# Optimization experiments

Measured on AMD Instinct MI355X. Metric: run time of the kernel, lower is better.

The kernel has to match this reference:

```python
import jax, jax.numpy as jnp
import numpy as np

N = 50000      # nodes
E = 800000     # edges (avg degree 16)
IN = 128       # in_dim0
H = 96         # hidden_dim
BN_EPS = 1e-5
PN_SCALE = 20.0


def setup_inputs() -> dict:
    key = jax.random.key(0)
    ks = jax.random.split(key, 12)
    s_in = 1.0 / np.sqrt(IN)
    s_h = 1.0 / np.sqrt(H)
    return {
        "x": jax.random.normal(ks[0], (N, IN), jnp.float32),
        "edge_index": jax.random.randint(ks[1], (2, E), 0, N, jnp.int32),
        # mlp0: Linear(in_dim0 -> hidden)
        "W0": jax.random.uniform(ks[2], (H, IN), jnp.float32, -s_in, s_in),
        "b0": jax.random.uniform(ks[3], (H,), jnp.float32, -s_in, s_in),
        # GIN MLP layer 1: Linear(hidden -> hidden) + BatchNorm
        "W1": jax.random.uniform(ks[4], (H, H), jnp.float32, -s_h, s_h),
        "b1": jax.random.uniform(ks[5], (H,), jnp.float32, -s_h, s_h),
        "gamma": jnp.ones((H,), jnp.float32),
        "beta": jnp.zeros((H,), jnp.float32),
        # GIN MLP layer 2: Linear(hidden -> hidden)
        "W2": jax.random.uniform(ks[6], (H, H), jnp.float32, -s_h, s_h),
        "b2": jax.random.uniform(ks[7], (H,), jnp.float32, -s_h, s_h),
    }


def reference(x, edge_index, W0, b0, W1, b1, gamma, beta, W2, b2):
    # h0 = mlp0(x)
    h0 = x @ W0.T + b0                                   # [N, H]

    # GINConv (eps=0): z_i = h0_i + sum_{j->i} h0_j
    src, dst = edge_index[0], edge_index[1]
    agg = jax.ops.segment_sum(h0[src], dst, num_segments=N)  # [N, H]
    z = h0 + agg

    # GIN MLP (layer_num=2): Linear -> BatchNorm(train) -> ReLU -> Linear
    h = z @ W1.T + b1
    mean = h.mean(axis=0)
    var = h.var(axis=0)                                  # biased, like torch BN
    h = (h - mean) * jax.lax.rsqrt(var + BN_EPS) * gamma + beta
    h = jax.nn.relu(h)
    l1 = h @ W2.T + b2                                   # [N, H]

    # PairNorm 'PN-SCS', scale=20
    col_mean = l1.mean(axis=0)
    rownorm = jnp.sqrt(1e-6 + jnp.sum(l1 * l1, axis=1, keepdims=True))
    l1 = PN_SCALE * l1 / rownorm - col_mean

    return (l1, h0)
```

## Files before the change

kernel.cpp:

```cpp
#include <hip/hip_runtime.h>

#define NN 50000
#define IN_DIM 128
#define HD 96
#define BN_EPS 1e-5f
#define PN_SCALE 20.0f
#define SCAN_NB 196
#define NREP 4

using bf16x8 = __attribute__((ext_vector_type(8))) short;
using f32x4  = __attribute__((ext_vector_type(4))) float;

__device__ __forceinline__ float4 ld4(const float* p) { return *(const float4*)p; }
__device__ __forceinline__ float4 add4(float4 a, float4 b) {
    return make_float4(a.x + b.x, a.y + b.y, a.z + b.z, a.w + b.w);
}

__device__ __forceinline__ short bfr(float f) {
    unsigned u = __float_as_uint(f);
    unsigned r = u + 0x7fffu + ((u >> 16) & 1u);
    return (short)(r >> 16);
}
__device__ __forceinline__ bf16x8 cvt8(float4 a, float4 b) {
    bf16x8 r;
    r[0] = bfr(a.x); r[1] = bfr(a.y); r[2] = bfr(a.z); r[3] = bfr(a.w);
    r[4] = bfr(b.x); r[5] = bfr(b.y); r[6] = bfr(b.z); r[7] = bfr(b.w);
    return r;
}

__global__ void zero_kernel(float* stats, int* cnt) {
    int i = blockIdx.x * blockDim.x + threadIdx.x;
    if (i < 1024) stats[i] = 0.0f;
    int j = i - 1024;
    if (j >= 0 && j < NREP * NN) cnt[j] = 0;
}

template<int K, int MODE>
__global__ __launch_bounds__(256) void gemm_mfma(
    const float* A, const float* __restrict__ W, const float* __restrict__ bias,
    float* out, const float* __restrict__ scale, const float* __restrict__ shift,
    float* __restrict__ gsum, float* __restrict__ gsumsq,
    float* __restrict__ gcol, float* __restrict__ growss,
    const int* __restrict__ ei, int* __restrict__ hist_cnt, int E)
{
    constexpr int P     = K + 8;
    constexpr int NS    = K / 32;
    constexpr int KD4   = K / 4;
    constexpr int WITER = (96 * KD4) / 256;
    constexpr int WL_SH  = 96 * P;
    constexpr int WL_TOT = (20608 > WL_SH) ? 20608 : WL_SH;
    __shared__ short Wl[WL_TOT];

    const int t    = threadIdx.x;
    const int l    = t & 63;
    const int w    = t >> 6;
    const int l15  = l & 15;
    const int lh   = l >> 4;
    const int base = blockIdx.x * 64;

    const int  arow = base + w * 16 + l15;
    const bool aok  = arow < NN;
    const float* Ap = A + (size_t)arow * K + lh * 8;
    const float4 Z4 = make_float4(0.f, 0.f, 0.f, 0.f);

    float4 pa[2 * NS];
#pragma unroll
    for (int s = 0; s < NS; ++s) {
        pa[2 * s]     = aok ? ld4(Ap + s * 32)     : Z4;
        pa[2 * s + 1] = aok ? ld4(Ap + s * 32 + 4) : Z4;
    }
    float4 wv[WITER];
#pragma unroll
    for (int i = 0; i < WITER; ++i) {
        int c = t + i * 256;
        int row = c / KD4, kq = c - row * KD4;
        wv[i] = ld4(W + (size_t)row * K + kq * 4);
    }
    float4 scv[2 * NS], shv[2 * NS];
    if (MODE == 2) {
#pragma unroll
        for (int s = 0; s < 2 * NS; ++s) {
            scv[s] = ld4(scale + (s >> 1) * 32 + lh * 8 + (s & 1) * 4);
            shv[s] = ld4(shift + (s >> 1) * 32 + lh * 8 + (s & 1) * 4);
        }
    }

    if (MODE == 0) {
        int e0 = (blockIdx.x * 256 + t) * 4;
        if (e0 + 4 <= E) {
            int4 d4 = *(const int4*)(ei + E + e0);
            atomicAdd(&hist_cnt[0 * NN + d4.x], 1);
            atomicAdd(&hist_cnt[1 * NN + d4.y], 1);
            atomicAdd(&hist_cnt[2 * NN + d4.z], 1);
            atomicAdd(&hist_cnt[3 * NN + d4.w], 1);
        } else {
            for (int i = 0; i < 4; ++i) {
                int e = e0 + i;
                if (e < E) atomicAdd(&hist_cnt[(e & 3) * NN + ei[E + e]], 1);
            }
        }
    }

    bf16x8 af[NS];
#pragma unroll
    for (int s = 0; s < NS; ++s) {
        float4 q0 = pa[2 * s], q1 = pa[2 * s + 1];
        if (MODE == 2) {
            float4 sc0 = scv[2 * s], sh0 = shv[2 * s];
            float4 sc1 = scv[2 * s + 1], sh1 = shv[2 * s + 1];
            q0.x = fmaxf(q0.x * sc0.x + sh0.x, 0.f);
            q0.y = fmaxf(q0.y * sc0.y + sh0.y, 0.f);
            q0.z = fmaxf(q0.z * sc0.z + sh0.z, 0.f);
            q0.w = fmaxf(q0.w * sc0.w + sh0.w, 0.f);
            q1.x = fmaxf(q1.x * sc1.x + sh1.x, 0.f);
            q1.y = fmaxf(q1.y * sc1.y + sh1.y, 0.f);
            q1.z = fmaxf(q1.z * sc1.z + sh1.z, 0.f);
            q1.w = fmaxf(q1.w * sc1.w + sh1.w, 0.f);
        }
        af[s] = cvt8(q0, q1);
    }

#pragma unroll
    for (int i = 0; i < WITER; ++i) {
        int c = t + i * 256;
        int row = c / KD4, kq = c - row * KD4;
        short4 s4v;
        s4v.x = bfr(wv[i].x); s4v.y = bfr(wv[i].y);
        s4v.z = bfr(wv[i].z); s4v.w = bfr(wv[i].w);
        *(short4*)(Wl + row * P + kq * 4) = s4v;
    }
    __syncthreads();

    f32x4 acc[6];
#pragma unroll
    for (int n = 0; n < 6; ++n) acc[n] = (f32x4){0.f, 0.f, 0.f, 0.f};

#pragma unroll
    for (int s = 0; s < NS; ++s) {
        const short* wp = Wl + s * 32 + lh * 8;
#pragma unroll
        for (int n = 0; n < 6; ++n) {
            bf16x8 bf = *(const bf16x8*)(wp + (n * 16 + l15) * P);
            acc[n] = __builtin_amdgcn_mfma_f32_16x16x32_bf16(af[s], bf, acc[n], 0, 0, 0);
        }
    }

    float cv[6][4];
#pragma unroll
    for (int n = 0; n < 6; ++n) {
        float b = bias[n * 16 + l15];
#pragma unroll
        for (int r = 0; r < 4; ++r) cv[n][r] = acc[n][r] + b;
    }
    int crow[4]; bool cok[4];
#pragma unroll
    for (int r = 0; r < 4; ++r) {
        crow[r] = base + w * 16 + lh * 4 + r;
        cok[r]  = crow[r] < NN;
    }
#pragma unroll
    for (int r = 0; r < 4; ++r) {
        if (cok[r]) {
            float* o = out + (size_t)crow[r] * HD + l15;
#pragma unroll
            for (int n = 0; n < 6; ++n) o[n * 16] = cv[n][r];
        }
    }

    if (MODE == 1) {
        float s[6], q[6];
#pragma unroll
        for (int n = 0; n < 6; ++n) {
            s[n] = 0.f; q[n] = 0.f;
#pragma unroll
            for (int r = 0; r < 4; ++r) {
                float v = cok[r] ? cv[n][r] : 0.f;
                s[n] += v; q[n] += v * v;
            }
        }
#pragma unroll
        for (int n = 0; n < 6; ++n) {
            s[n] += __shfl_xor(s[n], 16); s[n] += __shfl_xor(s[n], 32);
            q[n] += __shfl_xor(q[n], 16); q[n] += __shfl_xor(q[n], 32);
        }
        __syncthreads();
        float* red0 = (float*)Wl;
        float* red1 = red0 + 384;
        if (lh == 0) {
#pragma unroll
            for (int n = 0; n < 6; ++n) {
                red0[w * 96 + n * 16 + l15] = s[n];
                red1[w * 96 + n * 16 + l15] = q[n];
            }
        }
        __syncthreads();
        if (t < HD) {
            float S = red0[t] + red0[96 + t] + red0[192 + t] + red0[288 + t];
            float Q = red1[t] + red1[96 + t] + red1[192 + t] + red1[288 + t];
            atomicAdd(&gsum[t], S);
            atomicAdd(&gsumsq[t], Q);
        }
    }

    if (MODE == 2) {
        float s[6];
#pragma unroll
        for (int n = 0; n < 6; ++n) {
            s[n] = 0.f;
#pragma unroll
            for (int r = 0; r < 4; ++r) s[n] += cok[r] ? cv[n][r] : 0.f;
        }
#pragma unroll
        for (int n = 0; n < 6; ++n) {
            s[n] += __shfl_xor(s[n], 16); s[n] += __shfl_xor(s[n], 32);
        }
        float rq[4];
#pragma unroll
        for (int r = 0; r < 4; ++r) {
            float v = 0.f;
#pragma unroll
            for (int n = 0; n < 6; ++n) v = fmaf(cv[n][r], cv[n][r], v);
            v += __shfl_xor(v, 1); v += __shfl_xor(v, 2);
            v += __shfl_xor(v, 4); v += __shfl_xor(v, 8);
            rq[r] = v;
        }
        __syncthreads();
        float* red0 = (float*)Wl;
        if (lh == 0) {
#pragma unroll
            for (int n = 0; n < 6; ++n) red0[w * 96 + n * 16 + l15] = s[n];
        }
        __syncthreads();
        if (t < HD) {
            float S = red0[t] + red0[96 + t] + red0[192 + t] + red0[288 + t];
            atomicAdd(&gcol[t], S);
        }
        if (l15 == 0) {
#pragma unroll
            for (int r = 0; r < 4; ++r)
                if (cok[r]) growss[crow[r]] = rq[r];
        }
    }
}

__global__ __launch_bounds__(256) void scan_part1(const int* __restrict__ cnt,
                                                  int* __restrict__ bsum) {
    __shared__ int sh[256];
    int i = blockIdx.x * 256 + threadIdx.x;
    int t = threadIdx.x;
    int v = 0;
    if (i < NN)
        v = cnt[i] + cnt[NN + i] + cnt[2 * NN + i] + cnt[3 * NN + i];
    sh[t] = v;
    __syncthreads();
    for (int off = 128; off > 0; off >>= 1) {
        if (t < off) sh[t] += sh[t + off];
        __syncthreads();
    }
    if (t == 0) bsum[blockIdx.x] = sh[0];
}

__global__ __launch_bounds__(256) void scan_part2(int* __restrict__ bsum) {
    __shared__ int sh[256];
    int t = threadIdx.x;
    int v = (t < SCAN_NB) ? bsum[t] : 0;
    sh[t] = v;
    __syncthreads();
    for (int off = 1; off < 256; off <<= 1) {
        int u = sh[t];
        if (t >= off) u += sh[t - off];
        __syncthreads();
        sh[t] = u;
        __syncthreads();
    }
    if (t < SCAN_NB) bsum[t] = sh[t] - v;
}

__global__ __launch_bounds__(256) void scan_part3(int* __restrict__ cnt,
                                                  const int* __restrict__ bsum,
                                                  int* __restrict__ rowptr) {
    __shared__ int sh[256];
    int i = blockIdx.x * 256 + threadIdx.x;
    int t = threadIdx.x;
    int c0 = 0, c1 = 0, c2 = 0, c3 = 0;
    if (i < NN) {
        c0 = cnt[i]; c1 = cnt[NN + i]; c2 = cnt[2 * NN + i]; c3 = cnt[3 * NN + i];
    }
    int v = c0 + c1 + c2 + c3;
    sh[t] = v;
    __syncthreads();
    for (int off = 1; off < 256; off <<= 1) {
        int u = sh[t];
        if (t >= off) u += sh[t - off];
        __syncthreads();
        sh[t] = u;
        __syncthreads();
    }
    int excl = sh[t] - v + bsum[blockIdx.x];
    if (i < NN) {
        rowptr[i] = excl;
        cnt[i]          = excl;
        cnt[NN + i]     = excl + c0;
        cnt[2 * NN + i] = excl + c0 + c1;
        cnt[3 * NN + i] = excl + c0 + c1 + c2;
    }
    if (i == NN - 1) rowptr[NN] = excl + v;
}

__global__ __launch_bounds__(256) void fill_kernel(const int* __restrict__ ei,
                                                   int* __restrict__ cursor,
                                                   int* __restrict__ srcs, int E) {
    int t2 = blockIdx.x * 256 + threadIdx.x;
    int e0 = t2 * 2;
    int src[2], dst[2], rep[2];
#pragma unroll
    for (int i = 0; i < 2; ++i) {
        int e = e0 + i;
        bool ok = e < E;
        dst[i] = ok ? ei[E + e] : -1;
        src[i] = ok ? ei[e] : 0;
        rep[i] = e & 3;
    }
    for (int pass = 0; pass < 7; ++pass) {
#pragma unroll
        for (int i = 0; i < 2; ++i) {
            if (dst[i] >= 0 && (dst[i] >> 13) == pass) {
                int slot = atomicAdd(&cursor[rep[i] * NN + dst[i]], 1);
                srcs[slot] = src[i];
            }
        }
    }
}

__global__ __launch_bounds__(192) void gather_kernel(
    const float* __restrict__ h0, const int* __restrict__ rowptr,
    const int* __restrict__ srcs, float* __restrict__ z)
{
    const int tid = threadIdx.x;
    const int rl  = tid / 24;
    const int c   = tid - rl * 24;
    const int row = blockIdx.x * 8 + rl;
    if (row >= NN) return;

    const int p0 = rowptr[row];
    const int p1 = rowptr[row + 1];

    float4 acc = ld4(h0 + (size_t)row * HD + c * 4);

    int p = p0;
    for (; p + 8 <= p1; p += 8) {
        int s0 = srcs[p + 0], s1 = srcs[p + 1], s2 = srcs[p + 2], s3 = srcs[p + 3];
        int s4 = srcs[p + 4], s5 = srcs[p + 5], s6 = srcs[p + 6], s7 = srcs[p + 7];
        float4 v0 = ld4(h0 + (size_t)s0 * HD + c * 4);
        float4 v1 = ld4(h0 + (size_t)s1 * HD + c * 4);
        float4 v2 = ld4(h0 + (size_t)s2 * HD + c * 4);
        float4 v3 = ld4(h0 + (size_t)s3 * HD + c * 4);
        float4 v4 = ld4(h0 + (size_t)s4 * HD + c * 4);
        float4 v5 = ld4(h0 + (size_t)s5 * HD + c * 4);
        float4 v6 = ld4(h0 + (size_t)s6 * HD + c * 4);
        float4 v7 = ld4(h0 + (size_t)s7 * HD + c * 4);
        acc = add4(acc, add4(add4(add4(v0, v1), add4(v2, v3)),
                             add4(add4(v4, v5), add4(v6, v7))));
    }
    for (; p + 4 <= p1; p += 4) {
        int s0 = srcs[p + 0], s1 = srcs[p + 1], s2 = srcs[p + 2], s3 = srcs[p + 3];
        float4 v0 = ld4(h0 + (size_t)s0 * HD + c * 4);
        float4 v1 = ld4(h0 + (size_t)s1 * HD + c * 4);
        float4 v2 = ld4(h0 + (size_t)s2 * HD + c * 4);
        float4 v3 = ld4(h0 + (size_t)s3 * HD + c * 4);
        acc = add4(acc, add4(add4(v0, v1), add4(v2, v3)));
    }
    for (; p < p1; ++p)
        acc = add4(acc, ld4(h0 + (size_t)srcs[p] * HD + c * 4));

    *(float4*)(z + (size_t)row * HD + c * 4) = acc;
}

__global__ void bn_finalize_kernel(const float* __restrict__ sum, const float* __restrict__ sumsq,
                                   const float* __restrict__ gamma, const float* __restrict__ beta,
                                   float* __restrict__ scale, float* __restrict__ shift)
{
    int f = threadIdx.x;
    if (f < HD) {
        float mean = sum[f] * (1.0f / NN);
        float var  = fmaxf(sumsq[f] * (1.0f / NN) - mean * mean, 0.0f);
        float rstd = rsqrtf(var + BN_EPS);
        float sc = rstd * gamma[f];
        scale[f] = sc;
        shift[f] = beta[f] - mean * sc;
    }
}

__global__ __launch_bounds__(256) void pn_kernel(float* l1, const float* __restrict__ colsum,
                                                 const float* __restrict__ rowss)
{
    int idx = blockIdx.x * 256 + threadIdx.x;
    if (idx >= NN * 24) return;
    int row = idx / 24;
    int q = idx - row * 24;
    float rs = rsqrtf(1e-6f + rowss[row]);
    float4 v = ld4(l1 + (size_t)idx * 4);
    float4 cm = ld4(colsum + q * 4);
    v.x = PN_SCALE * v.x * rs - cm.x * (1.0f / NN);
    v.y = PN_SCALE * v.y * rs - cm.y * (1.0f / NN);
    v.z = PN_SCALE * v.z * rs - cm.z * (1.0f / NN);
    v.w = PN_SCALE * v.w * rs - cm.w * (1.0f / NN);
    *(float4*)(l1 + (size_t)idx * 4) = v;
}

extern "C" void kernel_launch(void* const* d_in, const int* in_sizes, int n_in,
                              void* d_out, int out_size, void* d_ws, size_t ws_size,
                              hipStream_t stream) {
    const float* x     = (const float*)d_in[0];
    const int*   ei    = (const int*)d_in[1];
    const float* W0    = (const float*)d_in[2];
    const float* b0    = (const float*)d_in[3];
    const float* W1    = (const float*)d_in[4];
    const float* b1    = (const float*)d_in[5];
    const float* gamma = (const float*)d_in[6];
    const float* beta  = (const float*)d_in[7];
    const float* W2    = (const float*)d_in[8];
    const float* b2    = (const float*)d_in[9];

    float* out_l1 = (float*)d_out;
    float* out_h0 = out_l1 + (size_t)NN * HD;

    float* stats   = (float*)d_ws;
    float* s_sum   = stats;
    float* s_sumsq = stats + HD;
    float* s_col   = stats + 2 * HD;
    float* s_scale = stats + 288;
    float* s_shift = stats + 384;
    float* rowss = stats + 1024;
    int* cnt    = (int*)(rowss + NN);
    int* rowptr = cnt + NREP * NN;
    int* bsum   = rowptr + NN + 2;
    int* srcs   = bsum + 256;

    const int E = in_sizes[1] / 2;
    const int GB = (NN + 63) / 64;

    zero_kernel<<<(1024 + NREP * NN + 255) / 256, 256, 0, stream>>>(stats, cnt);
    gemm_mfma<IN_DIM, 0><<<GB, 256, 0, stream>>>(x, W0, b0, out_h0, nullptr, nullptr,
                                                 nullptr, nullptr, nullptr, nullptr,
                                                 ei, cnt, E);
    scan_part1<<<SCAN_NB, 256, 0, stream>>>(cnt, bsum);
    scan_part2<<<1, 256, 0, stream>>>(bsum);
    scan_part3<<<SCAN_NB, 256, 0, stream>>>(cnt, bsum, rowptr);
    fill_kernel<<<(E / 2 + 255) / 256, 256, 0, stream>>>(ei, cnt, srcs, E);
    gather_kernel<<<(NN + 7) / 8, 192, 0, stream>>>(out_h0, rowptr, srcs, out_l1);
    gemm_mfma<HD, 1><<<GB, 256, 0, stream>>>(out_l1, W1, b1, out_l1, nullptr, nullptr,
                                             s_sum, s_sumsq, nullptr, nullptr,
                                             nullptr, nullptr, 0);
    bn_finalize_kernel<<<1, 128, 0, stream>>>(s_sum, s_sumsq, gamma, beta, s_scale, s_shift);
    gemm_mfma<HD, 2><<<GB, 256, 0, stream>>>(out_l1, W2, b2, out_l1, s_scale, s_shift,
                                             nullptr, nullptr, s_col, rowss,
                                             nullptr, nullptr, 0);
    pn_kernel<<<(NN * 24 + 255) / 256, 256, 0, stream>>>(out_l1, s_col, rowss);
}
```

Before: 292.4 us.

## Stage GEMM output through LDS for float4 stores; single cursor array in CSR fill

The GEMM epilogue now writes its accumulator tile to shared memory and reads it back so that each thread stores whole rows as float4, replacing scattered 4-byte stores with coalesced vector stores. The reduction scratch moves to a separate LDS offset so it no longer needs the extra barrier. The CSR fill now uses one cursor per destination instead of four replicated cursors, which simplifies the scan's write-back but concentrates atomics on a single counter per node. The cost is an extra LDS round trip and two barriers in the GEMM kernel, plus more atomic contention in the fill.

```diff
diff --git a/kernel.cpp b/kernel.cpp
--- a/kernel.cpp
+++ b/kernel.cpp
@@ -158,12 +158,27 @@
         crow[r] = base + w * 16 + lh * 4 + r;
         cok[r]  = crow[r] < NN;
     }
-#pragma unroll
-    for (int r = 0; r < 4; ++r) {
-        if (cok[r]) {
-            float* o = out + (size_t)crow[r] * HD + l15;
-#pragma unroll
-            for (int n = 0; n < 6; ++n) o[n * 16] = cv[n][r];
+
+    __syncthreads();
+    float* Cl = (float*)Wl;
+#pragma unroll
+    for (int n = 0; n < 6; ++n)
+#pragma unroll
+        for (int r = 0; r < 4; ++r)
+            Cl[(w * 16 + lh * 4 + r) * 100 + n * 16 + l15] = cv[n][r];
+    __syncthreads();
+    {
+        int lrow = t >> 2;
+        int q4   = t & 3;
+        int grow = base + lrow;
+        if (grow < NN) {
+            float* o = out + (size_t)grow * HD;
+            const float* cr = Cl + lrow * 100;
+#pragma unroll
+            for (int k = 0; k < 6; ++k) {
+                int c4 = q4 + k * 4;
+                *(float4*)(o + c4 * 4) = *(const float4*)(cr + c4 * 4);
+            }
         }
     }
 
@@ -183,8 +198,7 @@
             s[n] += __shfl_xor(s[n], 16); s[n] += __shfl_xor(s[n], 32);
             q[n] += __shfl_xor(q[n], 16); q[n] += __shfl_xor(q[n], 32);
         }
-        __syncthreads();
-        float* red0 = (float*)Wl;
+        float* red0 = (float*)Wl + 6400;
         float* red1 = red0 + 384;
         if (lh == 0) {
 #pragma unroll
@@ -224,8 +238,7 @@
             v += __shfl_xor(v, 4); v += __shfl_xor(v, 8);
             rq[r] = v;
         }
-        __syncthreads();
-        float* red0 = (float*)Wl;
+        float* red0 = (float*)Wl + 6400;
         if (lh == 0) {
 #pragma unroll
             for (int n = 0; n < 6; ++n) red0[w * 96 + n * 16 + l15] = s[n];
@@ -282,11 +295,9 @@
     __shared__ int sh[256];
     int i = blockIdx.x * 256 + threadIdx.x;
     int t = threadIdx.x;
-    int c0 = 0, c1 = 0, c2 = 0, c3 = 0;
-    if (i < NN) {
-        c0 = cnt[i]; c1 = cnt[NN + i]; c2 = cnt[2 * NN + i]; c3 = cnt[3 * NN + i];
-    }
-    int v = c0 + c1 + c2 + c3;
+    int v = 0;
+    if (i < NN)
+        v = cnt[i] + cnt[NN + i] + cnt[2 * NN + i] + cnt[3 * NN + i];
     sh[t] = v;
     __syncthreads();
     for (int off = 1; off < 256; off <<= 1) {
@@ -297,13 +308,7 @@
         __syncthreads();
     }
     int excl = sh[t] - v + bsum[blockIdx.x];
-    if (i < NN) {
-        rowptr[i] = excl;
-        cnt[i]          = excl;
-        cnt[NN + i]     = excl + c0;
-        cnt[2 * NN + i] = excl + c0 + c1;
-        cnt[3 * NN + i] = excl + c0 + c1 + c2;
-    }
+    if (i < NN) { rowptr[i] = excl; cnt[i] = excl; }
     if (i == NN - 1) rowptr[NN] = excl + v;
 }
 
@@ -312,20 +317,19 @@
                                                    int* __restrict__ srcs, int E) {
     int t2 = blockIdx.x * 256 + threadIdx.x;
     int e0 = t2 * 2;
-    int src[2], dst[2], rep[2];
+    int src[2], dst[2];
 #pragma unroll
     for (int i = 0; i < 2; ++i) {
         int e = e0 + i;
         bool ok = e < E;
         dst[i] = ok ? ei[E + e] : -1;
         src[i] = ok ? ei[e] : 0;
-        rep[i] = e & 3;
     }
     for (int pass = 0; pass < 7; ++pass) {
 #pragma unroll
         for (int i = 0; i < 2; ++i) {
             if (dst[i] >= 0 && (dst[i] >> 13) == pass) {
-                int slot = atomicAdd(&cursor[rep[i] * NN + dst[i]], 1);
+                int slot = atomicAdd(&cursor[dst[i]], 1);
                 srcs[slot] = src[i];
             }
         }
```

Result: no change. 293.8 us (+0.5%).
